# Kernel tuning notes

Hardware: AMD Instinct MI355X
Metric: run time of the kernel (lower is better)

Reference implementation:

```python
import jax, jax.numpy as jnp
import numpy as np

EMBEDDING_DIM = 64
N_EMBEDDINGS = 512


def setup_inputs() -> dict:
    key = jax.random.key(0)
    k1, k2 = jax.random.split(key)
    inputs = jax.random.normal(k1, (32, 64, 64, 64), dtype=jnp.float32)  # NCHW, C==embedding_dim
    weight = jax.random.normal(k2, (N_EMBEDDINGS, EMBEDDING_DIM), dtype=jnp.float32)
    return {"inputs": inputs, "weight": weight}


def reference(inputs, weight):
    # NCHW -> NHWC, flatten to [N, D]
    x = jnp.transpose(inputs, (0, 2, 3, 1))  # [B, H, W, D]
    in_shape = x.shape
    flat = x.reshape(-1, EMBEDDING_DIM)  # [N, D]

    distances = (
        jnp.sum(flat * flat, axis=1, keepdims=True)
        + jnp.sum(weight * weight, axis=1)
        - 2.0 * flat @ weight.T
    )
    idx = jnp.argmin(distances, axis=1)  # [N]

    # one-hot @ weight is just a gather
    quantized = weight[idx].reshape(in_shape)  # [B, H, W, D]

    # commitment loss: mse(stop_grad(quantized), x)
    e_latent_loss = jnp.mean(jnp.square(jax.lax.stop_gradient(quantized) - x))

    # straight-through estimator
    quantized = x + jax.lax.stop_gradient(quantized - x)

    return jnp.transpose(quantized, (0, 3, 1, 2)), e_latent_loss
```

## Files before the change

### kernel.cpp

```cpp
#include <hip/hip_runtime.h>
#include <math.h>

typedef short bf16x8 __attribute__((ext_vector_type(8)));
typedef float f32x4 __attribute__((ext_vector_type(4)));

#define VQ_D 64
#define VQ_K 512
#define VQ_NQ 131072
#define VQ_TOTAL 8388608
#define NCK 8
#define TAU 8e-3f

typedef __attribute__((address_space(1))) void as1_void;
typedef __attribute__((address_space(3))) void as3_void;

__device__ __forceinline__ void gll16(const void* g, void* l) {
    __builtin_amdgcn_global_load_lds((as1_void*)(void*)g, (as3_void*)l, 16, 0, 0);
}
__device__ __forceinline__ void gll4(const void* g, void* l) {
    __builtin_amdgcn_global_load_lds((as1_void*)(void*)g, (as3_void*)l, 4, 0, 0);
}

__device__ __forceinline__ ushort bf16_rne(float f) {
    uint u = __builtin_bit_cast(uint, f);
    u += 0x7fffu + ((u >> 16) & 1u);
    return (ushort)(u >> 16);
}
__device__ __forceinline__ float bf16_to_f(ushort h) {
    uint u = ((uint)h) << 16;
    return __builtin_bit_cast(float, u);
}
__device__ __forceinline__ uint rne_top(float r) {
    uint t = __builtin_bit_cast(uint, r);
    return t + 0x7fffu + ((t >> 16) & 1u);
}
__device__ __forceinline__ uint pack_hi16(uint a, uint b) {
    return __builtin_amdgcn_perm(b, a, 0x07060302u);
}

__global__ __launch_bounds__(128) void vq_prep(const float* __restrict__ w,
                                               ushort* __restrict__ wfrag,
                                               float* __restrict__ wn,
                                               float* __restrict__ out) {
    if (blockIdx.x == 0 && threadIdx.x == 0) out[VQ_TOTAL] = 0.f;
    const int tid = threadIdx.x;
    const int k = (blockIdx.x << 4) + (tid >> 3);
    const int g = tid & 7;
    const float4* row = (const float4*)(w + k * VQ_D);
    float4 a = row[2 * g], b4 = row[2 * g + 1];
    float v[8] = {a.x, a.y, a.z, a.w, b4.x, b4.y, b4.z, b4.w};
    ushort hi[8], lo[8];
    float nrm = 0.f;
#pragma unroll
    for (int j = 0; j < 8; ++j) {
        nrm = fmaf(v[j], v[j], nrm);
        hi[j] = bf16_rne(v[j]);
        lo[j] = bf16_rne(v[j] - bf16_to_f(hi[j]));
    }
    nrm += __shfl_xor(nrm, 1, 64);
    nrm += __shfl_xor(nrm, 2, 64);
    nrm += __shfl_xor(nrm, 4, 64);
    if (g == 0) wn[k] = nrm;
    const int t = k >> 4, col = k & 15;
    const int quad = g & 3, fh = g >> 2;
    bf16x8* basez = (bf16x8*)wfrag + t * 256 + quad * 16 + col;
    basez[fh * 64]       = *(bf16x8*)hi;
    basez[(2 + fh) * 64] = *(bf16x8*)lo;
}

__global__ __launch_bounds__(512, 8) void vq_main(const float* __restrict__ in,
                                                  const float* __restrict__ w,
                                                  const ushort* __restrict__ wfrag,
                                                  const float* __restrict__ wng,
                                                  float* __restrict__ out) {
    __shared__ __align__(16) char bstage[2][16384];
    __shared__ float wn_lds[VQ_K];
    __shared__ float xn_lds[128];
    __shared__ float best_lds[128], sec_lds[128];
    __shared__ int   bi_lds[128], si_lds[128];
    __shared__ double loss_lds[8];

    const int tid  = threadIdx.x;
    const int lane = tid & 63;
    const int wid  = tid >> 6;
    const int col  = lane & 15;
    const int quad = lane >> 4;
    const int n0  = blockIdx.x * 128;
    const int b   = n0 >> 12;
    const int hw0 = n0 & 4095;
    const float* xg0 = in + (b << 18) + hw0;

    {
        const char* gs = (const char*)wfrag + tid * 16;
        char* lb = &bstage[0][0] + wid * 1024;
        gll16(gs, lb);
        gll16(gs + 8192, lb + 8192);
        gll4(wng + tid, (char*)wn_lds + wid * 256);
    }

    bf16x8 ah0, ah1, al0, al1;
    {
        const float* xq = xg0 + wid * 16 + col;
        float sx = 0.f;
        uint AH0[4], AL0[4], AH1[4], AL1[4];
#pragma unroll
        for (int m = 0; m < 4; ++m) {
            float a0 = xq[(quad * 8 + 2 * m) << 12];
            float b0 = xq[(quad * 8 + 2 * m + 1) << 12];
            float a1 = xq[(32 + quad * 8 + 2 * m) << 12];
            float b1 = xq[(32 + quad * 8 + 2 * m + 1) << 12];
            sx = fmaf(a0, a0, sx); sx = fmaf(b0, b0, sx);
            sx = fmaf(a1, a1, sx); sx = fmaf(b1, b1, sx);
            uint ua0 = __builtin_bit_cast(uint, a0), ub0 = __builtin_bit_cast(uint, b0);
            uint ua1 = __builtin_bit_cast(uint, a1), ub1 = __builtin_bit_cast(uint, b1);
            AH0[m] = pack_hi16(ua0, ub0);
            AH1[m] = pack_hi16(ua1, ub1);
            float ha0 = __builtin_bit_cast(float, ua0 & 0xFFFF0000u);
            float hb0 = __builtin_bit_cast(float, ub0 & 0xFFFF0000u);
            float ha1 = __builtin_bit_cast(float, ua1 & 0xFFFF0000u);
            float hb1 = __builtin_bit_cast(float, ub1 & 0xFFFF0000u);
            AL0[m] = pack_hi16(rne_top(a0 - ha0), rne_top(b0 - hb0));
            AL1[m] = pack_hi16(rne_top(a1 - ha1), rne_top(b1 - hb1));
        }
        ah0 = *(bf16x8*)AH0; al0 = *(bf16x8*)AL0;
        ah1 = *(bf16x8*)AH1; al1 = *(bf16x8*)AL1;
        sx += __shfl_xor(sx, 16, 64);
        sx += __shfl_xor(sx, 32, 64);
        if (quad == 0) xn_lds[wid * 16 + col] = sx;
    }

    __syncthreads();

    float best[4], sec[4];
#pragma unroll
    for (int r = 0; r < 4; ++r) { best[r] = 3.0e38f; sec[r] = 3.0e38f; }

#pragma unroll 1
    for (int c = 0; c < NCK; ++c) {
        char* const bcur = &bstage[c & 1][0];
        if (c + 1 < NCK) {
            const char* gs = (const char*)wfrag + (c + 1) * 16384 + tid * 16;
            char* lb = &bstage[(c + 1) & 1][0] + wid * 1024;
            gll16(gs, lb);
            gll16(gs + 8192, lb + 8192);
        }
#pragma unroll
        for (int s = 0; s < 4; ++s) {
            const int t2 = 4 * c + s;
            const char* rb = bcur + s * 4096 + lane * 16;
            bf16x8 bh0 = *(const bf16x8*)(rb);
            bf16x8 bh1 = *(const bf16x8*)(rb + 1024);
            bf16x8 bl0 = *(const bf16x8*)(rb + 2048);
            bf16x8 bl1 = *(const bf16x8*)(rb + 3072);
            const float wnv = wn_lds[t2 * 16 + col];
            f32x4 acc = {0.f, 0.f, 0.f, 0.f};
            __builtin_amdgcn_s_setprio(1);
            acc = __builtin_amdgcn_mfma_f32_16x16x32_bf16(ah0, bh0, acc, 0, 0, 0);
            acc = __builtin_amdgcn_mfma_f32_16x16x32_bf16(ah1, bh1, acc, 0, 0, 0);
            acc = __builtin_amdgcn_mfma_f32_16x16x32_bf16(ah0, bl0, acc, 0, 0, 0);
            acc = __builtin_amdgcn_mfma_f32_16x16x32_bf16(ah1, bl1, acc, 0, 0, 0);
            acc = __builtin_amdgcn_mfma_f32_16x16x32_bf16(al0, bh0, acc, 0, 0, 0);
            acc = __builtin_amdgcn_mfma_f32_16x16x32_bf16(al1, bh1, acc, 0, 0, 0);
            __builtin_amdgcn_s_setprio(0);
#pragma unroll
            for (int j = 0; j < 4; ++j) {
                float dist = fmaf(-2.f, acc[j], wnv);
                uint u = (__builtin_bit_cast(uint, dist) & 0xFFFFFFE0u)
                       | ((uint)t2 & 0x1Fu);
                float key = __builtin_bit_cast(float, u);
                float m = fmaxf(best[j], key);
                best[j] = fminf(best[j], key);
                sec[j]  = fminf(sec[j], m);
            }
        }
        __syncthreads();
    }

    float bD[4], sD[4];
    int bI[4], sI[4];
#pragma unroll
    for (int r = 0; r < 4; ++r) {
        uint ub = __builtin_bit_cast(uint, best[r]);
        uint us = __builtin_bit_cast(uint, sec[r]);
        bI[r] = (int)(ub & 31u) * 16 + col;
        sI[r] = (int)(us & 31u) * 16 + col;
        bD[r] = __builtin_bit_cast(float, ub & 0xFFFFFFE0u);
        sD[r] = __builtin_bit_cast(float, us & 0xFFFFFFE0u);
    }

#pragma unroll
    for (int off = 1; off < 16; off <<= 1) {
#pragma unroll
        for (int r = 0; r < 4; ++r) {
            float ob = __shfl_xor(bD[r], off, 64);
            float os = __shfl_xor(sD[r], off, 64);
            int   oi = __shfl_xor(bI[r], off, 64);
            int   oc = __shfl_xor(sI[r], off, 64);
            bool oWins = (ob < bD[r]) || (ob == bD[r] && oi < bI[r]);
            float nb  = oWins ? ob    : bD[r];
            int   ni  = oWins ? oi    : bI[r];
            float c1  = oWins ? bD[r] : ob;
            int   ci1 = oWins ? bI[r] : oi;
            float c2  = oWins ? os    : sD[r];
            int   ci2 = oWins ? oc    : sI[r];
            bool c1w = (c1 < c2) || (c1 == c2 && ci1 < ci2);
            sD[r] = c1w ? c1  : c2;
            sI[r] = c1w ? ci1 : ci2;
            bD[r] = nb; bI[r] = ni;
        }
    }
    if (col == 0) {
#pragma unroll
        for (int r = 0; r < 4; ++r) {
            const int q = wid * 16 + quad * 4 + r;
            best_lds[q] = bD[r]; sec_lds[q] = sD[r];
            bi_lds[q] = bI[r];   si_lds[q] = sI[r];
        }
    }
    __syncthreads();

    {
        const int q = tid >> 2, part = tid & 3;
        float cb = best_lds[q], cs = sec_lds[q];
        int cbi = bi_lds[q], csi = si_lds[q];
        double chosen = (double)cb;
        if (cs - cb < TAU) {
            const float* wb  = w + cbi * VQ_D + part * 16;
            const float* ws2 = w + csi * VQ_D + part * 16;
            const float* xqp = xg0 + q;
            double nb = 0.0, dotb = 0.0, ns = 0.0, dots = 0.0;
#pragma unroll
            for (int d0 = 0; d0 < 16; ++d0) {
                const int d = part * 16 + d0;
                double xv = (double)xqp[d << 12];
                double wbv = (double)wb[d0], wsv = (double)ws2[d0];
                nb = fma(wbv, wbv, nb); dotb = fma(xv, wbv, dotb);
                ns = fma(wsv, wsv, ns); dots = fma(xv, wsv, dots);
            }
#pragma unroll
            for (int off = 1; off < 4; off <<= 1) {
                nb   += __shfl_xor(nb,   off, 64);
                dotb += __shfl_xor(dotb, off, 64);
                ns   += __shfl_xor(ns,   off, 64);
                dots += __shfl_xor(dots, off, 64);
            }
            double db = nb - 2.0 * dotb, ds = ns - 2.0 * dots;
            if (ds < db || (ds == db && csi < cbi)) { cbi = csi; chosen = ds; }
            else                                    { chosen = db; }
        }
        if (part == 0) bi_lds[q] = cbi;
        double lq = (part == 0) ? ((double)xn_lds[q] + chosen) : 0.0;
#pragma unroll
        for (int off = 32; off > 0; off >>= 1)
            lq += __shfl_down(lq, off, 64);
        if (lane == 0) loss_lds[wid] = lq;
    }
    __syncthreads();
    if (tid == 0) {
        double s = 0.0;
#pragma unroll
        for (int wv = 0; wv < 8; ++wv) s += loss_lds[wv];
        atomicAdd(out + VQ_TOTAL, (float)(s * (1.0 / (double)VQ_TOTAL)));
    }

    {
        const int q = tid & 127, quarter = tid >> 7;
        const float4* wrow = (const float4*)(w + bi_lds[q] * VQ_D) + quarter * 4;
        float* op = out + (b << 18) + hw0 + q;
#pragma unroll
        for (int u = 0; u < 4; ++u) {
            float4 v = wrow[u];
            const int d = quarter * 16 + 4 * u;
            op[(d + 0) << 12] = v.x;
            op[(d + 1) << 12] = v.y;
            op[(d + 2) << 12] = v.z;
            op[(d + 3) << 12] = v.w;
        }
    }
}

extern "C" void kernel_launch(void* const* d_in, const int* in_sizes, int n_in,
                              void* d_out, int out_size, void* d_ws, size_t ws_size,
                              hipStream_t stream) {
    const float* in = (const float*)d_in[0];
    const float* w  = (const float*)d_in[1];
    float* out = (float*)d_out;

    ushort* wfrag = (ushort*)d_ws;
    float*  wn    = (float*)((char*)d_ws + 131072);

    vq_prep<<<32, 128, 0, stream>>>(w, wfrag, wn, out);
    vq_main<<<VQ_NQ / 128, 512, 0, stream>>>(in, w, wfrag, wn, out);
}
```

Before: 116.6 us.

## Split codebook across wave pairs, each wave handling two query tiles

Each wave now covers 32 queries (two 16-query tiles) and half of each codebook chunk, where before it covered 16 queries and the whole chunk. Every B fragment read from LDS is reused across two MFMA chains, which halves LDS reads per MFMA. The top-2 candidates from the two codebook halves are merged through LDS before refinement. The cost is more registers, with launch bounds lowered from 8 to 6, and an extra merge step.

```diff
diff --git a/kernel.cpp b/kernel.cpp
--- a/kernel.cpp
+++ b/kernel.cpp
@@ -68,7 +68,7 @@
     basez[(2 + fh) * 64] = *(bf16x8*)lo;
 }
 
-__global__ __launch_bounds__(512, 8) void vq_main(const float* __restrict__ in,
+__global__ __launch_bounds__(512, 6) void vq_main(const float* __restrict__ in,
                                                   const float* __restrict__ w,
                                                   const ushort* __restrict__ wfrag,
                                                   const float* __restrict__ wng,
@@ -76,13 +76,16 @@
     __shared__ __align__(16) char bstage[2][16384];
     __shared__ float wn_lds[VQ_K];
     __shared__ float xn_lds[128];
-    __shared__ float best_lds[128], sec_lds[128];
-    __shared__ int   bi_lds[128], si_lds[128];
+    __shared__ float pb_lds[2][128], ps_lds[2][128];
+    __shared__ int   pi_lds[2][128], pj_lds[2][128];
+    __shared__ int   bi_lds[128];
     __shared__ double loss_lds[8];
 
     const int tid  = threadIdx.x;
     const int lane = tid & 63;
     const int wid  = tid >> 6;
+    const int qg   = wid >> 1;
+    const int cg   = wid & 1;
     const int col  = lane & 15;
     const int quad = lane >> 4;
     const int n0  = blockIdx.x * 128;
@@ -98,9 +101,10 @@
         gll4(wng + tid, (char*)wn_lds + wid * 256);
     }
 
-    bf16x8 ah0, ah1, al0, al1;
-    {
-        const float* xq = xg0 + wid * 16 + col;
+    bf16x8 ah0[2], ah1[2], al0[2], al1[2];
+#pragma unroll
+    for (int T = 0; T < 2; ++T) {
+        const float* xq = xg0 + qg * 32 + T * 16 + col;
         float sx = 0.f;
         uint AH0[4], AL0[4], AH1[4], AL1[4];
 #pragma unroll
@@ -122,18 +126,20 @@
             AL0[m] = pack_hi16(rne_top(a0 - ha0), rne_top(b0 - hb0));
             AL1[m] = pack_hi16(rne_top(a1 - ha1), rne_top(b1 - hb1));
         }
-        ah0 = *(bf16x8*)AH0; al0 = *(bf16x8*)AL0;
-        ah1 = *(bf16x8*)AH1; al1 = *(bf16x8*)AL1;
+        ah0[T] = *(bf16x8*)AH0; al0[T] = *(bf16x8*)AL0;
+        ah1[T] = *(bf16x8*)AH1; al1[T] = *(bf16x8*)AL1;
         sx += __shfl_xor(sx, 16, 64);
         sx += __shfl_xor(sx, 32, 64);
-        if (quad == 0) xn_lds[wid * 16 + col] = sx;
+        if (quad == 0) xn_lds[qg * 32 + T * 16 + col] = sx;
     }
 
     __syncthreads();
 
-    float best[4], sec[4];
-#pragma unroll
-    for (int r = 0; r < 4; ++r) { best[r] = 3.0e38f; sec[r] = 3.0e38f; }
+    float best[2][4], sec[2][4];
+#pragma unroll
+    for (int T = 0; T < 2; ++T)
+#pragma unroll
+        for (int r = 0; r < 4; ++r) { best[T][r] = 3.0e38f; sec[T][r] = 3.0e38f; }
 
 #pragma unroll 1
     for (int c = 0; c < NCK; ++c) {
@@ -145,84 +151,103 @@
             gll16(gs + 8192, lb + 8192);
         }
 #pragma unroll
-        for (int s = 0; s < 4; ++s) {
-            const int t2 = 4 * c + s;
-            const char* rb = bcur + s * 4096 + lane * 16;
+        for (int s = 0; s < 2; ++s) {
+            const int st = cg * 2 + s;
+            const int t2 = 4 * c + st;
+            const char* rb = bcur + st * 4096 + lane * 16;
             bf16x8 bh0 = *(const bf16x8*)(rb);
             bf16x8 bh1 = *(const bf16x8*)(rb + 1024);
             bf16x8 bl0 = *(const bf16x8*)(rb + 2048);
             bf16x8 bl1 = *(const bf16x8*)(rb + 3072);
             const float wnv = wn_lds[t2 * 16 + col];
-            f32x4 acc = {0.f, 0.f, 0.f, 0.f};
-            __builtin_amdgcn_s_setprio(1);
-            acc = __builtin_amdgcn_mfma_f32_16x16x32_bf16(ah0, bh0, acc, 0, 0, 0);
-            acc = __builtin_amdgcn_mfma_f32_16x16x32_bf16(ah1, bh1, acc, 0, 0, 0);
-            acc = __builtin_amdgcn_mfma_f32_16x16x32_bf16(ah0, bl0, acc, 0, 0, 0);
-            acc = __builtin_amdgcn_mfma_f32_16x16x32_bf16(ah1, bl1, acc, 0, 0, 0);
-            acc = __builtin_amdgcn_mfma_f32_16x16x32_bf16(al0, bh0, acc, 0, 0, 0);
-            acc = __builtin_amdgcn_mfma_f32_16x16x32_bf16(al1, bh1, acc, 0, 0, 0);
-            __builtin_amdgcn_s_setprio(0);
-#pragma unroll
-            for (int j = 0; j < 4; ++j) {
-                float dist = fmaf(-2.f, acc[j], wnv);
-                uint u = (__builtin_bit_cast(uint, dist) & 0xFFFFFFE0u)
-                       | ((uint)t2 & 0x1Fu);
-                float key = __builtin_bit_cast(float, u);
-                float m = fmaxf(best[j], key);
-                best[j] = fminf(best[j], key);
-                sec[j]  = fminf(sec[j], m);
+#pragma unroll
+            for (int T = 0; T < 2; ++T) {
+                f32x4 acc = {0.f, 0.f, 0.f, 0.f};
+                __builtin_amdgcn_s_setprio(1);
+                acc = __builtin_amdgcn_mfma_f32_16x16x32_bf16(ah0[T], bh0, acc, 0, 0, 0);
+                acc = __builtin_amdgcn_mfma_f32_16x16x32_bf16(ah1[T], bh1, acc, 0, 0, 0);
+                acc = __builtin_amdgcn_mfma_f32_16x16x32_bf16(ah0[T], bl0, acc, 0, 0, 0);
+                acc = __builtin_amdgcn_mfma_f32_16x16x32_bf16(ah1[T], bl1, acc, 0, 0, 0);
+                acc = __builtin_amdgcn_mfma_f32_16x16x32_bf16(al0[T], bh0, acc, 0, 0, 0);
+                acc = __builtin_amdgcn_mfma_f32_16x16x32_bf16(al1[T], bh1, acc, 0, 0, 0);
+                __builtin_amdgcn_s_setprio(0);
+#pragma unroll
+                for (int j = 0; j < 4; ++j) {
+                    float dist = fmaf(-2.f, acc[j], wnv);
+                    uint u = (__builtin_bit_cast(uint, dist) & 0xFFFFFFE0u)
+                           | ((uint)t2 & 0x1Fu);
+                    float key = __builtin_bit_cast(float, u);
+                    float m = fmaxf(best[T][j], key);
+                    best[T][j] = fminf(best[T][j], key);
+                    sec[T][j]  = fminf(sec[T][j], m);
+                }
             }
         }
         __syncthreads();
     }
 
-    float bD[4], sD[4];
-    int bI[4], sI[4];
+    float bD[2][4], sD[2][4];
+    int bI[2][4], sI[2][4];
+#pragma unroll
+    for (int T = 0; T < 2; ++T)
 #pragma unroll
     for (int r = 0; r < 4; ++r) {
-        uint ub = __builtin_bit_cast(uint, best[r]);
-        uint us = __builtin_bit_cast(uint, sec[r]);
-        bI[r] = (int)(ub & 31u) * 16 + col;
-        sI[r] = (int)(us & 31u) * 16 + col;
-        bD[r] = __builtin_bit_cast(float, ub & 0xFFFFFFE0u);
-        sD[r] = __builtin_bit_cast(float, us & 0xFFFFFFE0u);
+        uint ub = __builtin_bit_cast(uint, best[T][r]);
+        uint us = __builtin_bit_cast(uint, sec[T][r]);
+        bI[T][r] = (int)(ub & 31u) * 16 + col;
+        sI[T][r] = (int)(us & 31u) * 16 + col;
+        bD[T][r] = __builtin_bit_cast(float, ub & 0xFFFFFFE0u);
+        sD[T][r] = __builtin_bit_cast(float, us & 0xFFFFFFE0u);
     }
 
 #pragma unroll
     for (int off = 1; off < 16; off <<= 1) {
 #pragma unroll
+        for (int T = 0; T < 2; ++T)
+#pragma unroll
         for (int r = 0; r < 4; ++r) {
-            float ob = __shfl_xor(bD[r], off, 64);
-            float os = __shfl_xor(sD[r], off, 64);
-            int   oi = __shfl_xor(bI[r], off, 64);
-            int   oc = __shfl_xor(sI[r], off, 64);
-            bool oWins = (ob < bD[r]) || (ob == bD[r] && oi < bI[r]);
-            float nb  = oWins ? ob    : bD[r];
-            int   ni  = oWins ? oi    : bI[r];
-            float c1  = oWins ? bD[r] : ob;
-            int   ci1 = oWins ? bI[r] : oi;
-            float c2  = oWins ? os    : sD[r];
-            int   ci2 = oWins ? oc    : sI[r];
+            float ob = __shfl_xor(bD[T][r], off, 64);
+            float os = __shfl_xor(sD[T][r], off, 64);
+            int   oi = __shfl_xor(bI[T][r], off, 64);
+            int   oc = __shfl_xor(sI[T][r], off, 64);
+            bool oWins = (ob < bD[T][r]) || (ob == bD[T][r] && oi < bI[T][r]);
+            float nb  = oWins ? ob       : bD[T][r];
+            int   ni  = oWins ? oi       : bI[T][r];
+            float c1  = oWins ? bD[T][r] : ob;
+            int   ci1 = oWins ? bI[T][r] : oi;
+            float c2  = oWins ? os       : sD[T][r];
+            int   ci2 = oWins ? oc       : sI[T][r];
             bool c1w = (c1 < c2) || (c1 == c2 && ci1 < ci2);
-            sD[r] = c1w ? c1  : c2;
-            sI[r] = c1w ? ci1 : ci2;
-            bD[r] = nb; bI[r] = ni;
+            sD[T][r] = c1w ? c1  : c2;
+            sI[T][r] = c1w ? ci1 : ci2;
+            bD[T][r] = nb; bI[T][r] = ni;
         }
     }
     if (col == 0) {
 #pragma unroll
+        for (int T = 0; T < 2; ++T)
+#pragma unroll
         for (int r = 0; r < 4; ++r) {
-            const int q = wid * 16 + quad * 4 + r;
-            best_lds[q] = bD[r]; sec_lds[q] = sD[r];
-            bi_lds[q] = bI[r];   si_lds[q] = sI[r];
+            const int q = qg * 32 + T * 16 + quad * 4 + r;
+            pb_lds[cg][q] = bD[T][r]; ps_lds[cg][q] = sD[T][r];
+            pi_lds[cg][q] = bI[T][r]; pj_lds[cg][q] = sI[T][r];
         }
     }
     __syncthreads();
 
     {
         const int q = tid >> 2, part = tid & 3;
-        float cb = best_lds[q], cs = sec_lds[q];
-        int cbi = bi_lds[q], csi = si_lds[q];
+        float b0 = pb_lds[0][q], b1 = pb_lds[1][q];
+        float s0 = ps_lds[0][q], s1 = ps_lds[1][q];
+        int   i0 = pi_lds[0][q], i1 = pi_lds[1][q];
+        int   j0 = pj_lds[0][q], j1 = pj_lds[1][q];
+        bool w0 = (b0 < b1) || (b0 == b1 && i0 < i1);
+        float cb  = w0 ? b0 : b1;  int cbi = w0 ? i0 : i1;
+        float c1  = w0 ? b1 : b0;  int ci1 = w0 ? i1 : i0;
+        float c2  = w0 ? s0 : s1;  int ci2 = w0 ? j0 : j1;
+        bool c1w = (c1 < c2) || (c1 == c2 && ci1 < ci2);
+        float cs  = c1w ? c1 : c2; int csi = c1w ? ci1 : ci2;
+
         double chosen = (double)cb;
         if (cs - cb < TAU) {
             const float* wb  = w + cbi * VQ_D + part * 16;
```

New measurement: 187.8 us. 61.0% more time.
